# Kernel tuning notes

Hardware: AMD Instinct MI355X
Metric: run time of the kernel (lower is better)

Reference implementation:

```python
import jax, jax.numpy as jnp
import numpy as np

B, L, IDIM = 1, 1024, 2048
H, DK, DV, K = 16, 128, 128, 4
KEY_DIM = H * DK          # 2048
VAL_DIM = H * DV          # 2048
CONV_DIM = 2 * KEY_DIM + VAL_DIM  # 6144
EPS = 1e-6


def setup_inputs() -> dict:
    key = jax.random.key(0)
    ks = jax.random.split(key, 8)
    s = 0.02
    x = jax.random.normal(ks[0], (B, L, IDIM), jnp.float32)
    Wqkv = jax.random.normal(ks[1], (IDIM, CONV_DIM), jnp.float32) * s
    Wz = jax.random.normal(ks[2], (IDIM, VAL_DIM), jnp.float32) * s
    Wb = jax.random.normal(ks[3], (IDIM, H), jnp.float32) * s
    Wa = jax.random.normal(ks[4], (IDIM, H), jnp.float32) * s
    conv_w = jax.random.normal(ks[5], (CONV_DIM, 1, K), jnp.float32) * 0.2  # depthwise [O,I/g=1,K]
    A_log = jnp.log(jax.random.uniform(ks[6], (H,), jnp.float32, 0.1, 16.0))
    dt_bias = jnp.ones((H,), jnp.float32)
    norm_w = jnp.ones((DV,), jnp.float32)
    Wout = jax.random.normal(ks[7], (VAL_DIM, IDIM), jnp.float32) * s
    return dict(x=x, Wqkv=Wqkv, Wz=Wz, Wb=Wb, Wa=Wa, conv_w=conv_w,
                A_log=A_log, dt_bias=dt_bias, norm_w=norm_w, Wout=Wout)


def _l2norm(t):
    return t * jax.lax.rsqrt(jnp.sum(t * t, axis=-1, keepdims=True) + EPS)


def reference(x, Wqkv, Wz, Wb, Wa, conv_w, A_log, dt_bias, norm_w, Wout):
    b, l, _ = x.shape
    # fused QKV projection + causal depthwise conv + SiLU
    qkv = jnp.einsum('bld,dc->blc', x, Wqkv)                 # [B,L,CONV_DIM]
    qkv = jnp.transpose(qkv, (0, 2, 1))                      # [B,C,L]
    qkv = jax.lax.conv_general_dilated(
        qkv, conv_w, window_strides=(1,), padding=[(K - 1, 0)],
        dimension_numbers=('NCL', 'OIL', 'NCL'), feature_group_count=CONV_DIM)
    qkv = jax.nn.silu(jnp.transpose(qkv, (0, 2, 1)))         # [B,L,C]
    q, k, v = jnp.split(qkv, [KEY_DIM, 2 * KEY_DIM], axis=-1)

    z = jnp.einsum('bld,dv->blv', x, Wz)                     # [B,L,VAL_DIM]
    beta = jax.nn.sigmoid(jnp.einsum('bld,dh->blh', x, Wb))  # [B,L,H]
    A = -jnp.exp(A_log)                                      # [H]
    dt = jax.nn.softplus(jnp.einsum('bld,dh->blh', x, Wa) + dt_bias)
    g = dt * A                                               # [B,L,H] (negative)

    q = _l2norm(q.reshape(b, l, H, DK))
    k = _l2norm(k.reshape(b, l, H, DK))
    v = v.reshape(b, l, H, DV)
    scale = DK ** -0.5

    # time-major for scan: [L,B,H,...]
    qs = jnp.transpose(q, (1, 0, 2, 3)) * scale
    ks_ = jnp.transpose(k, (1, 0, 2, 3))
    vs = jnp.transpose(v, (1, 0, 2, 3))
    bs = jnp.transpose(beta, (1, 0, 2))
    gs = jnp.transpose(g, (1, 0, 2))

    M0 = jnp.zeros((b, H, DK, DV), jnp.float32)

    def step(M, inp):
        q_t, k_t, v_t, b_t, g_t = inp
        M = M * jnp.exp(g_t)[..., None, None]                    # decay
        Mk = jnp.einsum('bhd,bhdv->bhv', k_t, M)                 # readout of old mem
        M = M + jnp.einsum('bhd,bhv->bhdv', k_t, (v_t - Mk) * b_t[..., None])
        o_t = jnp.einsum('bhd,bhdv->bhv', q_t, M)
        return M, o_t

    _, out = jax.lax.scan(step, M0, (qs, ks_, vs, bs, gs))   # out: [L,B,H,DV]
    out = jnp.transpose(out, (1, 0, 2, 3))                   # [B,L,H,DV]

    # RMSNormGated: rms_norm(o) * weight * silu(z)
    zg = z.reshape(b, l, H, DV)
    rms = jax.lax.rsqrt(jnp.mean(out * out, axis=-1, keepdims=True) + EPS)
    out = (out * rms) * norm_w * jax.nn.silu(zg)

    out = out.reshape(b, l, VAL_DIM)
    return jnp.einsum('blv,vd->bld', out, Wout)
```

## Files before the change

### kernel.cpp

```cpp
#include <hip/hip_runtime.h>

typedef short bf16x8 __attribute__((ext_vector_type(8)));
typedef float f32x4 __attribute__((ext_vector_type(4)));
typedef float f32x2 __attribute__((ext_vector_type(2)));
typedef unsigned short u16;
typedef u16 u16x4 __attribute__((ext_vector_type(4)));

#define L_SEQ 1024
#define IDIM_ 2048
#define H_ 16
#define DK_ 128
#define DV_ 128
#define KEYD 2048
#define VALD 2048
#define CONVD 6144
#define QZD 8192
#define CH 16
#define NCH (L_SEQ / CH)

__device__ __forceinline__ u16 f2bf(float f) {
  union { float f; unsigned u; } v; v.f = f;
  unsigned r = v.u + 0x7FFF + ((v.u >> 16) & 1);
  return (u16)(r >> 16);
}

__device__ __forceinline__ float red16(float x) {
  union U { float f; int i; } a, t;
  a.f = x;
  t.i = __builtin_amdgcn_update_dpp(0, a.i, 0xB1, 0xF, 0xF, true); a.f += t.f;
  t.i = __builtin_amdgcn_update_dpp(0, a.i, 0x4E, 0xF, 0xF, true); a.f += t.f;
  t.i = __builtin_amdgcn_update_dpp(0, a.i, 0x141, 0xF, 0xF, true); a.f += t.f;
  t.i = __builtin_amdgcn_update_dpp(0, a.i, 0x140, 0xF, 0xF, true); a.f += t.f;
  return a.f;
}

__device__ __forceinline__ void gl_lds16(const float* g, float* l) {
  __builtin_amdgcn_global_load_lds(
      (const __attribute__((address_space(1))) void*)g,
      (__attribute__((address_space(3))) void*)l, 16, 0, 0);
}
__device__ __forceinline__ void gl_lds4(const float* g, float* l) {
  __builtin_amdgcn_global_load_lds(
      (const __attribute__((address_space(1))) void*)g,
      (__attribute__((address_space(3))) void*)l, 4, 0, 0);
}

__global__ __launch_bounds__(256) void prepcast_kernel(const float* __restrict__ x,
                                                       const float* __restrict__ Wqkv,
                                                       const float* __restrict__ Wz,
                                                       const float* __restrict__ Wout,
                                                       u16* __restrict__ xb,
                                                       u16* __restrict__ WcatT,
                                                       u16* __restrict__ WoutT) {
  __shared__ float tile[32][33];
  const int bid = blockIdx.x;
  if (bid < 2048) {
    int i = (bid * 256 + threadIdx.x) * 4;
    f32x4 v = *(const f32x4*)&x[i];
    u16x4 o = { f2bf(v[0]), f2bf(v[1]), f2bf(v[2]), f2bf(v[3]) };
    *(u16x4*)&xb[i] = o;
    return;
  }
  const float* W; u16* WT; int R, C, bx, by;
  if (bid < 14336) {
    int t = bid - 2048;  bx = t % 192; by = t / 192;
    W = Wqkv; WT = WcatT; R = IDIM_; C = CONVD;
  } else if (bid < 18432) {
    int t = bid - 14336; bx = t & 63; by = t >> 6;
    W = Wz; WT = WcatT + (size_t)CONVD * IDIM_; R = IDIM_; C = VALD;
  } else {
    int t = bid - 18432; bx = t & 63; by = t >> 6;
    W = Wout; WT = WoutT; R = VALD; C = IDIM_;
  }
  int c0 = bx * 32, r0 = by * 32;
  int tx = threadIdx.x & 31, ty = threadIdx.x >> 5;
#pragma unroll
  for (int j = 0; j < 4; ++j)
    tile[ty + j * 8][tx] = W[(size_t)(r0 + ty + j * 8) * C + c0 + tx];
  __syncthreads();
#pragma unroll
  for (int j = 0; j < 4; ++j)
    WT[(size_t)(c0 + ty + j * 8) * R + r0 + tx] = f2bf(tile[tx][ty + j * 8]);
}

__global__ __launch_bounds__(256) void gemm_bt_kernel(const u16* __restrict__ A,
                                                      const u16* __restrict__ B,
                                                      float* __restrict__ C,
                                                      int M, int N, int K) {
  __shared__ short As[128 * 72];
  __shared__ short Bs[128 * 72];
  const int tid = threadIdx.x;
  const int lane = tid & 63, wave = tid >> 6;
  const int wm = wave >> 1, wn = wave & 1;
  const int m0 = blockIdx.y * 128, n0 = blockIdx.x * 128;
  const int l15 = lane & 15, lhi = lane >> 4;

  f32x4 acc[4][4] = {};

  for (int k0 = 0; k0 < K; k0 += 64) {
    __syncthreads();
#pragma unroll
    for (int i = 0; i < 4; ++i) {
      int chunk = tid + i * 256;
      int row = chunk >> 3;
      int kc = (chunk & 7) * 8;
      *(bf16x8*)&As[row * 72 + kc] =
          *(const bf16x8*)&A[(size_t)(m0 + row) * K + k0 + kc];
      *(bf16x8*)&Bs[row * 72 + kc] =
          *(const bf16x8*)&B[(size_t)(n0 + row) * K + k0 + kc];
    }
    __syncthreads();
#pragma unroll
    for (int kk = 0; kk < 64; kk += 32) {
      const int koff = kk + lhi * 8;
      bf16x8 a[4], b[4];
#pragma unroll
      for (int m = 0; m < 4; ++m)
        a[m] = *(const bf16x8*)&As[(wm * 64 + m * 16 + l15) * 72 + koff];
#pragma unroll
      for (int n = 0; n < 4; ++n)
        b[n] = *(const bf16x8*)&Bs[(wn * 64 + n * 16 + l15) * 72 + koff];
#pragma unroll
      for (int m = 0; m < 4; ++m)
#pragma unroll
        for (int n = 0; n < 4; ++n)
          acc[m][n] = __builtin_amdgcn_mfma_f32_16x16x32_bf16(a[m], b[n], acc[m][n], 0, 0, 0);
    }
  }
#pragma unroll
  for (int m = 0; m < 4; ++m)
#pragma unroll
    for (int n = 0; n < 4; ++n)
#pragma unroll
      for (int j = 0; j < 4; ++j) {
        int row = m0 + wm * 64 + m * 16 + lhi * 4 + j;
        int col = n0 + wn * 64 + n * 16 + l15;
        C[(size_t)row * N + col] = acc[m][n][j];
      }
}

__global__ __launch_bounds__(256) void gemm_bt64_kernel(const u16* __restrict__ A,
                                                        const u16* __restrict__ B,
                                                        float* __restrict__ C,
                                                        int M, int N, int K) {
  __shared__ short As[64 * 72];
  __shared__ short Bs[128 * 72];
  const int tid = threadIdx.x;
  const int lane = tid & 63, wave = tid >> 6;
  const int wm = wave >> 1, wn = wave & 1;
  const int m0 = blockIdx.y * 64, n0 = blockIdx.x * 128;
  const int l15 = lane & 15, lhi = lane >> 4;

  f32x4 acc[2][4] = {};

  for (int k0 = 0; k0 < K; k0 += 64) {
    __syncthreads();
#pragma unroll
    for (int i = 0; i < 2; ++i) {
      int chunk = tid + i * 256;
      int row = chunk >> 3;
      int kc = (chunk & 7) * 8;
      *(bf16x8*)&As[row * 72 + kc] =
          *(const bf16x8*)&A[(size_t)(m0 + row) * K + k0 + kc];
    }
#pragma unroll
    for (int i = 0; i < 4; ++i) {
      int chunk = tid + i * 256;
      int row = chunk >> 3;
      int kc = (chunk & 7) * 8;
      *(bf16x8*)&Bs[row * 72 + kc] =
          *(const bf16x8*)&B[(size_t)(n0 + row) * K + k0 + kc];
    }
    __syncthreads();
#pragma unroll
    for (int kk = 0; kk < 64; kk += 32) {
      const int koff = kk + lhi * 8;
      bf16x8 a[2], b[4];
#pragma unroll
      for (int m = 0; m < 2; ++m)
        a[m] = *(const bf16x8*)&As[(wm * 32 + m * 16 + l15) * 72 + koff];
#pragma unroll
      for (int n = 0; n < 4; ++n)
        b[n] = *(const bf16x8*)&Bs[(wn * 64 + n * 16 + l15) * 72 + koff];
#pragma unroll
      for (int m = 0; m < 2; ++m)
#pragma unroll
        for (int n = 0; n < 4; ++n)
          acc[m][n] = __builtin_amdgcn_mfma_f32_16x16x32_bf16(a[m], b[n], acc[m][n], 0, 0, 0);
    }
  }
#pragma unroll
  for (int m = 0; m < 2; ++m)
#pragma unroll
    for (int n = 0; n < 4; ++n)
#pragma unroll
      for (int j = 0; j < 4; ++j) {
        int row = m0 + wm * 32 + m * 16 + lhi * 4 + j;
        int col = n0 + wn * 64 + n * 16 + l15;
        C[(size_t)row * N + col] = acc[m][n][j];
      }
}

__global__ __launch_bounds__(128) void betag_kernel(const float* __restrict__ x,
                                                    const float* __restrict__ Wb,
                                                    const float* __restrict__ Wa,
                                                    const float* __restrict__ A_log,
                                                    const float* __restrict__ dt_bias,
                                                    float* __restrict__ btT,
                                                    float* __restrict__ egT) {
  int l = blockIdx.x;
  __shared__ float xs[IDIM_];
  __shared__ float redb[128], reda[128];
  for (int i = threadIdx.x; i < IDIM_; i += 128) xs[i] = x[(size_t)l * IDIM_ + i];
  __syncthreads();
  int h = threadIdx.x & 15, part = threadIdx.x >> 4;
  float sb = 0.f, sa = 0.f;
  int d0 = part * 256;
  for (int d = d0; d < d0 + 256; ++d) {
    float xv = xs[d];
    sb += xv * Wb[d * 16 + h];
    sa += xv * Wa[d * 16 + h];
  }
  redb[threadIdx.x] = sb;
  reda[threadIdx.x] = sa;
  __syncthreads();
  if (threadIdx.x < 16) {
    float b = 0.f, a = 0.f;
#pragma unroll
    for (int p = 0; p < 8; ++p) { b += redb[p * 16 + h]; a += reda[p * 16 + h]; }
    btT[h * L_SEQ + l] = 1.f / (1.f + expf(-b));
    float dtv = a + dt_bias[h];
    dtv = (dtv > 20.f) ? dtv : log1pf(expf(dtv));
    float g = -expf(A_log[h]) * dtv;
    egT[h * L_SEQ + l] = expf(g);
  }
}

__global__ __launch_bounds__(256) void prep2_kernel(const float* __restrict__ qkvz,
                                                    const float* __restrict__ cw,
                                                    float* __restrict__ qn,
                                                    float* __restrict__ kn,
                                                    float* __restrict__ qkT,
                                                    float* __restrict__ vT) {
  __shared__ float tile[32][33];
  const int bid = blockIdx.x;
  if (bid < 4096) {
    int wid = bid * 4 + (threadIdx.x >> 6);
    int lane = threadIdx.x & 63;
    int l = wid >> 4, h = wid & 15;
    const int cq = h * 128 + lane * 2;
    const int ck = KEYD + cq;
    const float* row0 = qkvz + (size_t)l * QZD;
    f32x4 wq0 = *(const f32x4*)&cw[cq * 4];
    f32x4 wq1 = *(const f32x4*)&cw[(cq + 1) * 4];
    f32x4 wk0 = *(const f32x4*)&cw[ck * 4];
    f32x4 wk1 = *(const f32x4*)&cw[(ck + 1) * 4];
    f32x2 xq = *(const f32x2*)&row0[cq];
    f32x2 xk = *(const f32x2*)&row0[ck];
    float q0 = xq[0] * wq0[3], q1 = xq[1] * wq1[3];
    float k0 = xk[0] * wk0[3], k1 = xk[1] * wk1[3];
    if (l >= 1) {
      f32x2 aq = *(const f32x2*)&row0[cq - QZD];
      f32x2 ak = *(const f32x2*)&row0[ck - QZD];
      q0 += aq[0] * wq0[2]; q1 += aq[1] * wq1[2];
      k0 += ak[0] * wk0[2]; k1 += ak[1] * wk1[2];
    }
    if (l >= 2) {
      f32x2 aq = *(const f32x2*)&row0[cq - 2 * QZD];
      f32x2 ak = *(const f32x2*)&row0[ck - 2 * QZD];
      q0 += aq[0] * wq0[1]; q1 += aq[1] * wq1[1];
      k0 += ak[0] * wk0[1]; k1 += ak[1] * wk1[1];
    }
    if (l >= 3) {
      f32x2 aq = *(const f32x2*)&row0[cq - 3 * QZD];
      f32x2 ak = *(const f32x2*)&row0[ck - 3 * QZD];
      q0 += aq[0] * wq0[0]; q1 += aq[1] * wq1[0];
      k0 += ak[0] * wk0[0]; k1 += ak[1] * wk1[0];
    }
    f32x2 qv = { q0 / (1.f + expf(-q0)), q1 / (1.f + expf(-q1)) };
    f32x2 kv = { k0 / (1.f + expf(-k0)), k1 / (1.f + expf(-k1)) };

    float ssq = qv[0] * qv[0] + qv[1] * qv[1];
    float ssk = kv[0] * kv[0] + kv[1] * kv[1];
#pragma unroll
    for (int s = 1; s < 64; s <<= 1) {
      ssq += __shfl_xor(ssq, s);
      ssk += __shfl_xor(ssk, s);
    }
    float scq = 0.08838834764831845f / sqrtf(ssq + 1e-6f);
    float sck = 1.f / sqrtf(ssk + 1e-6f);
    qv[0] *= scq; qv[1] *= scq;
    kv[0] *= sck; kv[1] *= sck;
    size_t base = ((size_t)h * L_SEQ + l) * 128 + lane * 2;
    *(f32x2*)&qn[base] = qv;
    *(f32x2*)&kn[base] = kv;
    float qk = qv[0] * kv[0] + qv[1] * kv[1];
#pragma unroll
    for (int s = 1; s < 64; s <<= 1) qk += __shfl_xor(qk, s);
    if (lane == 0) qkT[h * L_SEQ + l] = qk;
    return;
  }
  int t = bid - 4096;
  int c0 = (t & 63) * 32, l0 = (t >> 6) * 32;
  int tx = threadIdx.x & 31, ty = threadIdx.x >> 5;
  const int c = 2 * KEYD + c0 + tx;
  f32x4 w = *(const f32x4*)&cw[c * 4];
#pragma unroll
  for (int j = 0; j < 4; ++j) {
    int l = l0 + ty + j * 8;
    const float* p = qkvz + (size_t)l * QZD + c;
    float s = p[0] * w[3];
    if (l >= 1) s += p[-QZD] * w[2];
    if (l >= 2) s += p[-2 * QZD] * w[1];
    if (l >= 3) s += p[-3 * QZD] * w[0];
    tile[ty + j * 8][tx] = s / (1.f + expf(-s));
  }
  __syncthreads();
#pragma unroll
  for (int j = 0; j < 4; ++j)
    vT[(size_t)(c0 + ty + j * 8) * L_SEQ + l0 + tx] = tile[tx][ty + j * 8];
}

__global__ __launch_bounds__(256) void scan_kernel(const float* __restrict__ qn,
                                                   const float* __restrict__ kn,
                                                   const float* __restrict__ vT,
                                                   const float* __restrict__ egT,
                                                   const float* __restrict__ btT,
                                                   const float* __restrict__ qkT,
                                                   float* __restrict__ oatt) {
  __shared__ alignas(16) float qs[2][CH][128];
  __shared__ alignas(16) float ks[2][CH][128];
  __shared__ alignas(16) float vs[2][16][CH];
  __shared__ alignas(16) float ebc[2][3][CH];

  const int tid = threadIdx.x;
  const int wave = tid >> 6, lane = tid & 63;
  const int dk_sub = lane & 15;
  const int head = blockIdx.x & 15;
  const int dv0 = (blockIdx.x >> 4) * 16;
  const int col_local = tid >> 4;
  const int dv = dv0 + col_local;

  const float* qh = qn + (size_t)head * L_SEQ * 128;
  const float* kh = kn + (size_t)head * L_SEQ * 128;

  auto stage = [&](int chunk, int buf) {
    const int l0 = chunk * CH;
    const float* qg = qh + (size_t)l0 * 128;
    const float* kg = kh + (size_t)l0 * 128;
#pragma unroll
    for (int i = 0; i < 2; ++i) {
      int seg = i * 4 + wave;
      int off = seg * 256 + lane * 4;
      gl_lds16(qg + off, &qs[buf][0][0] + seg * 256);
      gl_lds16(kg + off, &ks[buf][0][0] + seg * 256);
    }
    {
      int idx = wave * 64 + lane;
      gl_lds4(vT + (size_t)(head * 128 + dv0 + (idx >> 4)) * L_SEQ + l0 + (idx & 15),
              &vs[buf][0][0] + wave * 64);
    }
    if (wave == 0 && lane < 48) {
      const float* src = (lane < 16) ? (egT + head * L_SEQ + l0 + lane)
                       : (lane < 32) ? (btT + head * L_SEQ + l0 + (lane - 16))
                                     : (qkT + head * L_SEQ + l0 + (lane - 32));
      gl_lds4(src, &ebc[buf][0][0]);
    }
  };

  stage(0, 0);
  __syncthreads();

  f32x4 Mlo = {0.f, 0.f, 0.f, 0.f}, Mhi = {0.f, 0.f, 0.f, 0.f};
  const int dkb = dk_sub * 8;

#pragma unroll 1
  for (int c = 0; c < NCH; ++c) {
    const int buf = c & 1;
    if (c + 1 < NCH) stage(c + 1, buf ^ 1);

    f32x4 ev[4], bv[4], cv[4], vv[4];
#pragma unroll
    for (int i = 0; i < 4; ++i) {
      ev[i] = *(const f32x4*)&ebc[buf][0][i * 4];
      bv[i] = *(const f32x4*)&ebc[buf][1][i * 4];
      cv[i] = *(const f32x4*)&ebc[buf][2][i * 4];
      vv[i] = *(const f32x4*)&vs[buf][col_local][i * 4];
    }
    f32x4 qr[4][2], kr[4][2];
#pragma unroll
    for (int i = 0; i < 3; ++i) {
      qr[i][0] = *(const f32x4*)&qs[buf][i][dkb];
      qr[i][1] = *(const f32x4*)&qs[buf][i][dkb + 4];
      kr[i][0] = *(const f32x4*)&ks[buf][i][dkb];
      kr[i][1] = *(const f32x4*)&ks[buf][i][dkb + 4];
    }

#pragma unroll
    for (int s = 0; s < CH; ++s) {
      if (s + 3 < CH) {
        qr[(s + 3) & 3][0] = *(const f32x4*)&qs[buf][s + 3][dkb];
        qr[(s + 3) & 3][1] = *(const f32x4*)&qs[buf][s + 3][dkb + 4];
        kr[(s + 3) & 3][0] = *(const f32x4*)&ks[buf][s + 3][dkb];
        kr[(s + 3) & 3][1] = *(const f32x4*)&ks[buf][s + 3][dkb + 4];
      }
      const f32x4 q0 = qr[s & 3][0], q1 = qr[s & 3][1];
      const f32x4 k0 = kr[s & 3][0], k1 = kr[s & 3][1];
      const float e = ev[s >> 2][s & 3], b = bv[s >> 2][s & 3];
      const float qk = cv[s >> 2][s & 3], v = vv[s >> 2][s & 3];

      float skm0 = k0[0] * Mlo[0], skm1 = k0[1] * Mlo[1];
      float sqm0 = q0[0] * Mlo[0], sqm1 = q0[1] * Mlo[1];
      skm0 = fmaf(k0[2], Mlo[2], skm0); skm1 = fmaf(k0[3], Mlo[3], skm1);
      sqm0 = fmaf(q0[2], Mlo[2], sqm0); sqm1 = fmaf(q0[3], Mlo[3], sqm1);
      skm0 = fmaf(k1[0], Mhi[0], skm0); skm1 = fmaf(k1[1], Mhi[1], skm1);
      sqm0 = fmaf(q1[0], Mhi[0], sqm0); sqm1 = fmaf(q1[1], Mhi[1], sqm1);
      skm0 = fmaf(k1[2], Mhi[2], skm0); skm1 = fmaf(k1[3], Mhi[3], skm1);
      sqm0 = fmaf(q1[2], Mhi[2], sqm0); sqm1 = fmaf(q1[3], Mhi[3], sqm1);
      f32x4 emlo, emhi;
#pragma unroll
      for (int i = 0; i < 4; ++i) { emlo[i] = e * Mlo[i]; emhi[i] = e * Mhi[i]; }
      float skm = red16(skm0 + skm1);
      float sqm = red16(sqm0 + sqm1);
      float dl = (v - e * skm) * b;
      float o = fmaf(qk, dl, e * sqm);
      if (dk_sub == 0)
        oatt[(size_t)((c * CH + s) * 16 + head) * 128 + dv] = o;
#pragma unroll
      for (int i = 0; i < 4; ++i) {
        Mlo[i] = fmaf(k0[i], dl, emlo[i]);
        Mhi[i] = fmaf(k1[i], dl, emhi[i]);
      }
    }
    __syncthreads();
  }
}

__global__ __launch_bounds__(256) void grms_kernel(const float* __restrict__ oatt,
                                                   const float* __restrict__ qkvz,
                                                   const float* __restrict__ norm_w,
                                                   u16* __restrict__ gn) {
  int wid = blockIdx.x * 4 + (threadIdx.x >> 6);
  int lane = threadIdx.x & 63;
  int l = wid >> 4, h = wid & 15;
  const float* o = oatt + (size_t)wid * 128;
  f32x2 ov = *(const f32x2*)&o[lane * 2];
  float ss = ov[0] * ov[0] + ov[1] * ov[1];
#pragma unroll
  for (int s = 1; s < 64; s <<= 1) ss += __shfl_xor(ss, s);
  float r = 1.f / sqrtf(ss * (1.f / 128.f) + 1e-6f);
  const float* zp = qkvz + (size_t)l * QZD + CONVD + h * 128;
  f32x2 zv = *(const f32x2*)&zp[lane * 2];
  u16 r0, r1;
  {
    float sil = zv[0] / (1.f + expf(-zv[0]));
    r0 = f2bf(ov[0] * r * norm_w[lane * 2] * sil);
    float sil1 = zv[1] / (1.f + expf(-zv[1]));
    r1 = f2bf(ov[1] * r * norm_w[lane * 2 + 1] * sil1);
  }
  u16* dst = gn + (size_t)l * VALD + h * 128 + lane * 2;
  dst[0] = r0; dst[1] = r1;
}

extern "C" void kernel_launch(void* const* d_in, const int* in_sizes, int n_in,
                              void* d_out, int out_size, void* d_ws, size_t ws_size,
                              hipStream_t stream) {
  const float* x      = (const float*)d_in[0];
  const float* Wqkv   = (const float*)d_in[1];
  const float* Wz     = (const float*)d_in[2];
  const float* Wb     = (const float*)d_in[3];
  const float* Wa     = (const float*)d_in[4];
  const float* conv_w = (const float*)d_in[5];
  const float* A_log  = (const float*)d_in[6];
  const float* dt_bias= (const float*)d_in[7];
  const float* norm_w = (const float*)d_in[8];
  const float* Wout   = (const float*)d_in[9];
  float* out = (float*)d_out;

  char* ws = (char*)d_ws;
  size_t off = 0;
  auto alloc = [&](size_t bytes) {
    void* p = ws + off;
    off = (off + bytes + 255) & ~(size_t)255;
    return p;
  };
  u16* xb     = (u16*)alloc((size_t)L_SEQ * IDIM_ * 2);
  u16* WcatT  = (u16*)alloc((size_t)QZD * IDIM_ * 2);
  u16* WoutT  = (u16*)alloc((size_t)IDIM_ * VALD * 2);
  float* qkvz = (float*)alloc((size_t)L_SEQ * QZD * 4);
  float* qn   = (float*)alloc((size_t)H_ * L_SEQ * 128 * 4);
  float* kn   = (float*)alloc((size_t)H_ * L_SEQ * 128 * 4);
  float* vT   = (float*)alloc((size_t)H_ * 128 * L_SEQ * 4);
  float* btT  = (float*)alloc((size_t)L_SEQ * H_ * 4);
  float* egT  = (float*)alloc((size_t)L_SEQ * H_ * 4);
  float* qkTb = (float*)alloc((size_t)L_SEQ * H_ * 4);
  float* oatt = (float*)alloc((size_t)L_SEQ * H_ * DV_ * 4);
  u16* gn     = (u16*)alloc((size_t)L_SEQ * VALD * 2);

  prepcast_kernel<<<22528, 256, 0, stream>>>(x, Wqkv, Wz, Wout, xb, WcatT, WoutT);

  gemm_bt_kernel<<<dim3(QZD / 128, L_SEQ / 128), 256, 0, stream>>>(xb, WcatT, qkvz, L_SEQ, QZD, IDIM_);

  betag_kernel<<<L_SEQ, 128, 0, stream>>>(x, Wb, Wa, A_log, dt_bias, btT, egT);

  prep2_kernel<<<6144, 256, 0, stream>>>(qkvz, conv_w, qn, kn, qkTb, vT);

  scan_kernel<<<H_ * (DV_ / 16), 256, 0, stream>>>(qn, kn, vT, egT, btT, qkTb, oatt);

  grms_kernel<<<(L_SEQ * H_) / 4, 256, 0, stream>>>(oatt, qkvz, norm_w, gn);
  gemm_bt64_kernel<<<dim3(IDIM_ / 128, L_SEQ / 64), 256, 0, stream>>>(gn, WoutT, out, L_SEQ, IDIM_, VALD);
}
```

Measured before the change: 368.8 us.

## Split delta-rule scan into a state-only recurrence and a chunked parallel output pass

The sequential scan now computes only the delta term and the state update, with no per-step q readout or second cross-lane reduction. Every 64 steps it saves the memory state M to global memory. A new opass kernel then rebuilds outputs per 64-step chunk from that saved state, a causal decayed q·k matrix, and the stored deltas. This shortens the serial critical path of the recurrence, at the cost of an extra kernel, about 16MB of state checkpoint traffic, and unoptimized scalar FP32 loops in the output pass.

```diff
diff --git a/kernel.cpp b/kernel.cpp
--- a/kernel.cpp
+++ b/kernel.cpp
@@ -17,6 +17,8 @@
 #define QZD 8192
 #define CH 16
 #define NCH (L_SEQ / CH)
+#define SCH 64
+#define NSC (L_SEQ / SCH)
 
 __device__ __forceinline__ u16 f2bf(float f) {
   union { float f; unsigned u; } v; v.f = f;
@@ -207,7 +209,8 @@
                                                     const float* __restrict__ A_log,
                                                     const float* __restrict__ dt_bias,
                                                     float* __restrict__ btT,
-                                                    float* __restrict__ egT) {
+                                                    float* __restrict__ egT,
+                                                    float* __restrict__ gT) {
   int l = blockIdx.x;
   __shared__ float xs[IDIM_];
   __shared__ float redb[128], reda[128];
@@ -233,6 +236,7 @@
     dtv = (dtv > 20.f) ? dtv : log1pf(expf(dtv));
     float g = -expf(A_log[h]) * dtv;
     egT[h * L_SEQ + l] = expf(g);
+    gT[h * L_SEQ + l] = g;
   }
 }
 
@@ -321,17 +325,15 @@
     vT[(size_t)(c0 + ty + j * 8) * L_SEQ + l0 + tx] = tile[tx][ty + j * 8];
 }
 
-__global__ __launch_bounds__(256) void scan_kernel(const float* __restrict__ qn,
-                                                   const float* __restrict__ kn,
+__global__ __launch_bounds__(256) void scan_kernel(const float* __restrict__ kn,
                                                    const float* __restrict__ vT,
                                                    const float* __restrict__ egT,
                                                    const float* __restrict__ btT,
-                                                   const float* __restrict__ qkT,
-                                                   float* __restrict__ oatt) {
-  __shared__ alignas(16) float qs[2][CH][128];
+                                                   float* __restrict__ Mb,
+                                                   float* __restrict__ Db) {
   __shared__ alignas(16) float ks[2][CH][128];
   __shared__ alignas(16) float vs[2][16][CH];
-  __shared__ alignas(16) float ebc[2][3][CH];
+  __shared__ alignas(16) float ebc[2][2][CH];
 
   const int tid = threadIdx.x;
   const int wave = tid >> 6, lane = tid & 63;
@@ -341,18 +343,15 @@
   const int col_local = tid >> 4;
   const int dv = dv0 + col_local;
 
-  const float* qh = qn + (size_t)head * L_SEQ * 128;
   const float* kh = kn + (size_t)head * L_SEQ * 128;
 
   auto stage = [&](int chunk, int buf) {
     const int l0 = chunk * CH;
-    const float* qg = qh + (size_t)l0 * 128;
     const float* kg = kh + (size_t)l0 * 128;
 #pragma unroll
     for (int i = 0; i < 2; ++i) {
       int seg = i * 4 + wave;
       int off = seg * 256 + lane * 4;
-      gl_lds16(qg + off, &qs[buf][0][0] + seg * 256);
       gl_lds16(kg + off, &ks[buf][0][0] + seg * 256);
     }
     {
@@ -360,10 +359,9 @@
       gl_lds4(vT + (size_t)(head * 128 + dv0 + (idx >> 4)) * L_SEQ + l0 + (idx & 15),
               &vs[buf][0][0] + wave * 64);
     }
-    if (wave == 0 && lane < 48) {
+    if (wave == 0 && lane < 32) {
       const float* src = (lane < 16) ? (egT + head * L_SEQ + l0 + lane)
-                       : (lane < 32) ? (btT + head * L_SEQ + l0 + (lane - 16))
-                                     : (qkT + head * L_SEQ + l0 + (lane - 32));
+                                     : (btT + head * L_SEQ + l0 + (lane - 16));
       gl_lds4(src, &ebc[buf][0][0]);
     }
   };
@@ -379,19 +377,23 @@
     const int buf = c & 1;
     if (c + 1 < NCH) stage(c + 1, buf ^ 1);
 
-    f32x4 ev[4], bv[4], cv[4], vv[4];
+    if ((c & 3) == 0) {
+      int sc = c >> 2;
+      float* mrow = Mb + (((size_t)sc * 16 + head) * 128 + dv) * 128 + dkb;
+      *(f32x4*)mrow = Mlo;
+      *(f32x4*)(mrow + 4) = Mhi;
+    }
+
+    f32x4 ev[4], bv[4], vv[4];
 #pragma unroll
     for (int i = 0; i < 4; ++i) {
       ev[i] = *(const f32x4*)&ebc[buf][0][i * 4];
       bv[i] = *(const f32x4*)&ebc[buf][1][i * 4];
-      cv[i] = *(const f32x4*)&ebc[buf][2][i * 4];
       vv[i] = *(const f32x4*)&vs[buf][col_local][i * 4];
     }
-    f32x4 qr[4][2], kr[4][2];
+    f32x4 kr[4][2];
 #pragma unroll
     for (int i = 0; i < 3; ++i) {
-      qr[i][0] = *(const f32x4*)&qs[buf][i][dkb];
-      qr[i][1] = *(const f32x4*)&qs[buf][i][dkb + 4];
       kr[i][0] = *(const f32x4*)&ks[buf][i][dkb];
       kr[i][1] = *(const f32x4*)&ks[buf][i][dkb + 4];
     }
@@ -399,33 +401,24 @@
 #pragma unroll
     for (int s = 0; s < CH; ++s) {
       if (s + 3 < CH) {
-        qr[(s + 3) & 3][0] = *(const f32x4*)&qs[buf][s + 3][dkb];
-        qr[(s + 3) & 3][1] = *(const f32x4*)&qs[buf][s + 3][dkb + 4];
         kr[(s + 3) & 3][0] = *(const f32x4*)&ks[buf][s + 3][dkb];
         kr[(s + 3) & 3][1] = *(const f32x4*)&ks[buf][s + 3][dkb + 4];
       }
-      const f32x4 q0 = qr[s & 3][0], q1 = qr[s & 3][1];
       const f32x4 k0 = kr[s & 3][0], k1 = kr[s & 3][1];
       const float e = ev[s >> 2][s & 3], b = bv[s >> 2][s & 3];
-      const float qk = cv[s >> 2][s & 3], v = vv[s >> 2][s & 3];
+      const float v = vv[s >> 2][s & 3];
 
       float skm0 = k0[0] * Mlo[0], skm1 = k0[1] * Mlo[1];
-      float sqm0 = q0[0] * Mlo[0], sqm1 = q0[1] * Mlo[1];
       skm0 = fmaf(k0[2], Mlo[2], skm0); skm1 = fmaf(k0[3], Mlo[3], skm1);
-      sqm0 = fmaf(q0[2], Mlo[2], sqm0); sqm1 = fmaf(q0[3], Mlo[3], sqm1);
       skm0 = fmaf(k1[0], Mhi[0], skm0); skm1 = fmaf(k1[1], Mhi[1], skm1);
-      sqm0 = fmaf(q1[0], Mhi[0], sqm0); sqm1 = fmaf(q1[1], Mhi[1], sqm1);
       skm0 = fmaf(k1[2], Mhi[2], skm0); skm1 = fmaf(k1[3], Mhi[3], skm1);
-      sqm0 = fmaf(q1[2], Mhi[2], sqm0); sqm1 = fmaf(q1[3], Mhi[3], sqm1);
       f32x4 emlo, emhi;
 #pragma unroll
       for (int i = 0; i < 4; ++i) { emlo[i] = e * Mlo[i]; emhi[i] = e * Mhi[i]; }
       float skm = red16(skm0 + skm1);
-      float sqm = red16(sqm0 + sqm1);
       float dl = (v - e * skm) * b;
-      float o = fmaf(qk, dl, e * sqm);
       if (dk_sub == 0)
-        oatt[(size_t)((c * CH + s) * 16 + head) * 128 + dv] = o;
+        Db[(size_t)((c * CH + s) * 16 + head) * 128 + dv] = dl;
 #pragma unroll
       for (int i = 0; i < 4; ++i) {
         Mlo[i] = fmaf(k0[i], dl, emlo[i]);
@@ -433,6 +426,101 @@
       }
     }
     __syncthreads();
+  }
+}
+
+__global__ __launch_bounds__(256) void opass_kernel(const float* __restrict__ qn,
+                                                    const float* __restrict__ kn,
+                                                    const float* __restrict__ Db,
+                                                    const float* __restrict__ gT,
+                                                    const float* __restrict__ Mb,
+                                                    float* __restrict__ oatt) {
+  __shared__ alignas(16) float qs[SCH][128];
+  __shared__ alignas(16) float ks2[SCH][128];
+  __shared__ alignas(16) float ds[SCH][128];
+  __shared__ float As[SCH][SCH];
+  __shared__ float gsh[SCH], Gh[SCH];
+
+  const int tid = threadIdx.x, wave = tid >> 6, lane = tid & 63;
+  const int h = blockIdx.x & 15, sc = blockIdx.x >> 4;
+  const int l0 = sc * SCH;
+
+  const float* qg = qn + ((size_t)h * L_SEQ + l0) * 128;
+  const float* kg = kn + ((size_t)h * L_SEQ + l0) * 128;
+#pragma unroll
+  for (int i = 0; i < 8; ++i) {
+    int seg = i * 4 + wave;
+    int off = seg * 256 + lane * 4;
+    gl_lds16(qg + off, &qs[0][0] + seg * 256);
+    gl_lds16(kg + off, &ks2[0][0] + seg * 256);
+  }
+#pragma unroll
+  for (int j = 0; j < 32; ++j) {
+    int idx = tid + j * 256;
+    int t = idx >> 7, dv = idx & 127;
+    ds[t][dv] = Db[((size_t)(l0 + t) * 16 + h) * 128 + dv];
+  }
+  if (tid < SCH) gsh[tid] = gT[h * L_SEQ + l0 + tid];
+  __syncthreads();
+  if (tid < SCH) {
+    float a = 0.f;
+    for (int u = 0; u <= tid; ++u) a += gsh[u];
+    Gh[tid] = a;
+  }
+  __syncthreads();
+#pragma unroll
+  for (int j = 0; j < 16; ++j) {
+    int p = tid + j * 256;
+    int t = p >> 6, s = p & 63;
+    float a = 0.f;
+    if (s <= t) {
+      float acc = 0.f;
+      for (int d = 0; d < 128; d += 4) {
+        f32x4 q4 = *(const f32x4*)&qs[t][d];
+        f32x4 k4 = *(const f32x4*)&ks2[s][d];
+        acc += q4[0] * k4[0] + q4[1] * k4[1] + q4[2] * k4[2] + q4[3] * k4[3];
+      }
+      a = acc * expf(Gh[t] - Gh[s]);
+    }
+    As[t][s] = a;
+  }
+  __syncthreads();
+
+  const int dv = tid & 127, half = tid >> 7;
+  float o2a[32], o1a[32];
+#pragma unroll
+  for (int i = 0; i < 32; ++i) { o2a[i] = 0.f; o1a[i] = 0.f; }
+  for (int i = 0; i < 32; ++i) {
+    int t = half * 32 + i;
+    float acc = 0.f;
+    for (int s = 0; s <= t; ++s) acc = fmaf(As[t][s], ds[s][dv], acc);
+    o2a[i] = acc;
+  }
+  const float* mrow = Mb + (((size_t)sc * 16 + h) * 128 + dv) * 128;
+  for (int dc = 0; dc < 8; ++dc) {
+    f32x4 m0 = *(const f32x4*)&mrow[dc * 16];
+    f32x4 m1 = *(const f32x4*)&mrow[dc * 16 + 4];
+    f32x4 m2 = *(const f32x4*)&mrow[dc * 16 + 8];
+    f32x4 m3 = *(const f32x4*)&mrow[dc * 16 + 12];
+#pragma unroll
+    for (int i = 0; i < 32; ++i) {
+      int t = half * 32 + i;
+      f32x4 q0 = *(const f32x4*)&qs[t][dc * 16];
+      f32x4 q1 = *(const f32x4*)&qs[t][dc * 16 + 4];
+      f32x4 q2 = *(const f32x4*)&qs[t][dc * 16 + 8];
+      f32x4 q3 = *(const f32x4*)&qs[t][dc * 16 + 12];
+      float a = q0[0] * m0[0] + q0[1] * m0[1] + q0[2] * m0[2] + q0[3] * m0[3]
+              + q1[0] * m1[0] + q1[1] * m1[1] + q1[2] * m1[2] + q1[3] * m1[3]
+              + q2[0] * m2[0] + q2[1] * m2[1] + q2[2] * m2[2] + q2[3] * m2[3]
+              + q3[0] * m3[0] + q3[1] * m3[1] + q3[2] * m3[2] + q3[3] * m3[3];
+      o1a[i] += a;
+    }
+  }
+#pragma unroll
+  for (int i = 0; i < 32; ++i) {
+    int t = half * 32 + i;
+    float o = fmaf(expf(Gh[t]), o1a[i], o2a[i]);
+    oatt[((size_t)(l0 + t) * 16 + h) * 128 + dv] = o;
   }
 }
 
@@ -493,7 +581,10 @@
   float* vT   = (float*)alloc((size_t)H_ * 128 * L_SEQ * 4);
   float* btT  = (float*)alloc((size_t)L_SEQ * H_ * 4);
   float* egT  = (float*)alloc((size_t)L_SEQ * H_ * 4);
+  float* gTb  = (float*)alloc((size_t)L_SEQ * H_ * 4);
   float* qkTb = (float*)alloc((size_t)L_SEQ * H_ * 4);
+  float* Mb   = (float*)alloc((size_t)NSC * H_ * 128 * 128 * 4);
+  float* Db   = (float*)alloc((size_t)L_SEQ * H_ * DV_ * 4);
   float* oatt = (float*)alloc((size_t)L_SEQ * H_ * DV_ * 4);
   u16* gn     = (u16*)alloc((size_t)L_SEQ * VALD * 2);
 
@@ -501,11 +592,13 @@
 
   gemm_bt_kernel<<<dim3(QZD / 128, L_SEQ / 128), 256, 0, stream>>>(xb, WcatT, qkvz, L_SEQ, QZD, IDIM_);
 
-  betag_kernel<<<L_SEQ, 128, 0, stream>>>(x, Wb, Wa, A_log, dt_bias, btT, egT);
+  betag_kernel<<<L_SEQ, 128, 0, stream>>>(x, Wb, Wa, A_log, dt_bias, btT, egT, gTb);
 
   prep2_kernel<<<6144, 256, 0, stream>>>(qkvz, conv_w, qn, kn, qkTb, vT);
 
-  scan_kernel<<<H_ * (DV_ / 16), 256, 0, stream>>>(qn, kn, vT, egT, btT, qkTb, oatt);
+  scan_kernel<<<H_ * (DV_ / 16), 256, 0, stream>>>(kn, vT, egT, btT, Mb, Db);
+
+  opass_kernel<<<NSC * H_, 256, 0, stream>>>(qn, kn, Db, gTb, Mb, oatt);
 
   grms_kernel<<<(L_SEQ * H_) / 4, 256, 0, stream>>>(oatt, qkvz, norm_w, gn);
   gemm_bt64_kernel<<<dim3(IDIM_ / 128, L_SEQ / 64), 256, 0, stream>>>(gn, WoutT, out, L_SEQ, IDIM_, VALD);
```

Measured after the change: 414.0 us. 12.3% more time.
